# Performance work log

Measured on AMD Instinct MI355X. Metric: run time of the kernel, lower is better.

Reference implementation:

```python
import jax, jax.numpy as jnp
import numpy as np
from jax import lax

SPLINE_ORDER = 3  # default in KANLinear


def make_grid(in_features, grid_size, order=SPLINE_ORDER):
    # grid_range = [-1, 1], extended by spline_order knots on each side
    h = 2.0 / grid_size
    g = jnp.arange(-order, grid_size + order + 1, dtype=jnp.float32) * h - 1.0
    return jnp.broadcast_to(g, (in_features, g.shape[0]))  # (in, G)


def b_splines(x, grid, order=SPLINE_ORDER):
    # x: (N, in), grid: (in, G). Cox-de Boor recursion.
    x = x[..., None]  # (N, in, 1)
    bases = ((x >= grid[:, :-1]) & (x < grid[:, 1:])).astype(x.dtype)
    for k in range(1, order + 1):
        bases = ((x - grid[:, : -(k + 1)]) / (grid[:, k:-1] - grid[:, : -(k + 1)]) * bases[..., :-1]
                 + (grid[:, k + 1:] - x) / (grid[:, k + 1:] - grid[:, 1:-k]) * bases[..., 1:])
    return bases  # (N, in, grid_size + order)


def kan_conv(x, base_w, spline_w, scaler, grid_size, kernel, pad):
    # x: (B, C, H, W); base_w: (n_convs, K); spline_w: (n_convs, K, grid_size+order); scaler: (n_convs, K)
    B, C, H, W = x.shape
    kh, kw = kernel
    K = kh * kw
    if K == 1:
        p = x.reshape(-1, 1)  # (B*C*H*W, 1)
        Ho, Wo = H, W
    else:
        # patches: (B, C*K, Ho, Wo), feature dim ordered channel-major then (kh, kw)
        patches = lax.conv_general_dilated_patches(x, (kh, kw), (1, 1), [(pad, pad), (pad, pad)])
        Ho, Wo = patches.shape[2], patches.shape[3]
        p = patches.reshape(B, C, K, Ho, Wo).transpose(0, 1, 3, 4, 2).reshape(-1, K)
    grid = make_grid(K, grid_size)
    bases = b_splines(p, grid)  # (N, K, coef) -- shared across all n_convs kernels
    base = jnp.einsum('ni,ki->nk', jax.nn.silu(p), base_w)
    spl = jnp.einsum('nic,kic->nk', bases, spline_w * scaler[..., None])
    n_convs = base_w.shape[0]
    # channel ordering: each input channel expanded into n_convs outputs (channel-major)
    out = (base + spl).reshape(B, C, Ho, Wo, n_convs).transpose(0, 1, 4, 2, 3)
    return out.reshape(B, C * n_convs, Ho, Wo)


def setup_inputs() -> dict:
    key = jax.random.key(0)
    ks = jax.random.split(key, 12)
    B, C, H, W = 4, 3, 256, 256
    coef3 = 3 + SPLINE_ORDER  # grid_size=3 -> 6 spline coefficients
    coef5 = 5 + SPLINE_ORDER  # grid_size=5 (default, kan_conv6) -> 8
    s9 = 1.0 / np.sqrt(9.0)
    return {
        'x': jax.random.normal(ks[0], (B, C, H, W), jnp.float32),
        'base_w1': jax.random.normal(ks[1], (2, 9), jnp.float32) * s9,
        'spline_w1': jax.random.normal(ks[2], (2, 9, coef3), jnp.float32) * 0.1,
        'scaler1': 1.0 + 0.1 * jax.random.normal(ks[3], (2, 9), jnp.float32),
        'base_w2': jax.random.normal(ks[4], (2, 9), jnp.float32) * s9,
        'spline_w2': jax.random.normal(ks[5], (2, 9, coef3), jnp.float32) * 0.1,
        'scaler2': 1.0 + 0.1 * jax.random.normal(ks[6], (2, 9), jnp.float32),
        'conv_w': jax.random.normal(ks[7], (3, 12, 1, 1), jnp.float32) * (1.0 / np.sqrt(12.0)),
        'conv_b': jax.random.normal(ks[8], (3,), jnp.float32) * 0.01,
        'base_w6': jax.random.normal(ks[9], (1, 1), jnp.float32),
        'spline_w6': jax.random.normal(ks[10], (1, 1, coef5), jnp.float32) * 0.1,
        'scaler6': 1.0 + 0.1 * jax.random.normal(ks[11], (1, 1), jnp.float32),
    }


def reference(x, base_w1, spline_w1, scaler1, base_w2, spline_w2, scaler2,
              conv_w, conv_b, base_w6, spline_w6, scaler6):
    x = kan_conv(x, base_w1, spline_w1, scaler1, grid_size=3, kernel=(3, 3), pad=1)   # (B,6,H,W)
    x = kan_conv(x, base_w2, spline_w2, scaler2, grid_size=3, kernel=(3, 3), pad=1)   # (B,12,H,W)
    x = jnp.einsum('bchw,oc->bohw', x, conv_w[:, :, 0, 0]) + conv_b[None, :, None, None]  # 1x1 conv -> (B,3,H,W)
    return kan_conv(x, base_w6, spline_w6, scaler6, grid_size=5, kernel=(1, 1), pad=0)  # (B,3,H,W)
```

## Files before the change

### kernel.cpp

```cpp
#include <hip/hip_runtime.h>

#define TILE 16

__device__ __forceinline__ float2 kan_enc(float v, float g0, float invh, float tmax) {
    float g = v / (1.0f + __expf(-v));
    float T = (v - g0) * invh;
    float U = (T >= 0.0f && T < tmax) ? T : -1.0f;
    float2 r; r.x = g; r.y = U; return r;
}

__device__ __forceinline__ float poly_eval(float4 c, float w) {
    return ((c.w * w + c.z) * w + c.y) * w + c.x;
}

__global__ __launch_bounds__(256) void ZS_MKAN_72121090834671_kernel(
    const float* __restrict__ x,
    const float* __restrict__ base_w1, const float* __restrict__ spline_w1,
    const float* __restrict__ scaler1,
    const float* __restrict__ base_w2, const float* __restrict__ spline_w2,
    const float* __restrict__ scaler2,
    const float* __restrict__ conv_w, const float* __restrict__ conv_b,
    const float* __restrict__ base_w6, const float* __restrict__ spline_w6,
    const float* __restrict__ scaler6,
    float* __restrict__ out)
{
    __shared__ float2 encX[1200];
    __shared__ float2 encY[1944];
    __shared__ float4 coefL[2][2][9][10];
    __shared__ float4 coef6[12];
    __shared__ float  sbw[2][18];
    __shared__ float  scw[36], scb[3];
    __shared__ float  sb6;

    const int tid = threadIdx.x;
    const int tx0 = blockIdx.x * TILE;
    const int ty0 = blockIdx.y * TILE;
    const int b   = blockIdx.z;

    for (int e = tid; e < 360; e += 256) {
        int l = e / 180, r = e % 180, k = r / 90, r2 = r % 90, s = r2 / 10, si = r2 % 10;
        float4 v = make_float4(0.f, 0.f, 0.f, 0.f);
        if (si > 0) {
            const float* sw  = l ? spline_w2 : spline_w1;
            const float* scl = l ? scaler2   : scaler1;
            float sc = scl[k * 9 + s];
            int m = si - 1;
            float W[4];
            #pragma unroll
            for (int j = 0; j < 4; ++j) {
                int c = m - 3 + j;
                W[j] = (c >= 0 && c < 6) ? sw[(k * 9 + s) * 6 + c] * sc : 0.0f;
            }
            const float s6 = 1.0f / 6.0f;
            v.x = (W[0] + 4.0f * W[1] + W[2]) * s6;
            v.y = 3.0f * (W[2] - W[0]) * s6;
            v.z = (3.0f * W[0] - 6.0f * W[1] + 3.0f * W[2]) * s6;
            v.w = (W[3] - W[0] + 3.0f * (W[1] - W[2])) * s6;
        }
        coefL[l][k][s][si] = v;
    }
    if (tid < 12) {
        float4 v = make_float4(0.f, 0.f, 0.f, 0.f);
        if (tid > 0) {
            float sc = scaler6[0];
            int m = tid - 1;
            float W[4];
            #pragma unroll
            for (int j = 0; j < 4; ++j) {
                int c = m - 3 + j;
                W[j] = (c >= 0 && c < 8) ? spline_w6[c] * sc : 0.0f;
            }
            const float s6 = 1.0f / 6.0f;
            v.x = (W[0] + 4.0f * W[1] + W[2]) * s6;
            v.y = 3.0f * (W[2] - W[0]) * s6;
            v.z = (3.0f * W[0] - 6.0f * W[1] + 3.0f * W[2]) * s6;
            v.w = (W[3] - W[0] + 3.0f * (W[1] - W[2])) * s6;
        }
        coef6[tid] = v;
    }
    if (tid < 18) { sbw[0][tid] = base_w1[tid]; sbw[1][tid] = base_w2[tid]; }
    if (tid < 36) scw[tid] = conv_w[tid];
    if (tid < 3)  scb[tid] = conv_b[tid];
    if (tid == 0) sb6 = base_w6[0];

    for (int i = tid; i < 1200; i += 256) {
        int c = i / 400, r = i % 400, ly = r / 20, lx = r % 20;
        int gy = ty0 - 2 + ly, gx = tx0 - 2 + lx;
        float v = 0.0f;
        if ((unsigned)gy < 256u && (unsigned)gx < 256u)
            v = x[((b * 3 + c) * 256 + gy) * 256 + gx];
        encX[i] = kan_enc(v, -3.0f, 1.5f, 9.0f);
    }
    __syncthreads();

    for (int i = tid; i < 972; i += 256) {
        int c = i / 324, r = i % 324, ly = r / 18, lx = r % 18;
        float a0 = 0.0f, a1 = 0.0f;
        int base = c * 400 + ly * 20 + lx;
        #pragma unroll
        for (int s = 0; s < 9; ++s) {
            float2 t = encX[base + (s / 3) * 20 + (s % 3)];
            float mf = floorf(t.y);
            float w  = t.y - mf;
            int  si  = (int)mf + 1;
            a0 += t.x * sbw[0][s]     + poly_eval(coefL[0][0][s][si], w);
            a1 += t.x * sbw[0][9 + s] + poly_eval(coefL[0][1][s][si], w);
        }
        int gy = ty0 - 1 + ly, gx = tx0 - 1 + lx;
        if (!((unsigned)gy < 256u && (unsigned)gx < 256u)) { a0 = 0.0f; a1 = 0.0f; }
        encY[(c * 2 + 0) * 324 + r] = kan_enc(a0, -3.0f, 1.5f, 9.0f);
        encY[(c * 2 + 1) * 324 + r] = kan_enc(a1, -3.0f, 1.5f, 9.0f);
    }
    __syncthreads();

    const int ly = tid >> 4, lx = tid & 15;
    float z[12];
    #pragma unroll
    for (int c = 0; c < 6; ++c) {
        float a0 = 0.0f, a1 = 0.0f;
        int base = c * 324 + ly * 18 + lx;
        #pragma unroll
        for (int s = 0; s < 9; ++s) {
            float2 t = encY[base + (s / 3) * 18 + (s % 3)];
            float mf = floorf(t.y);
            float w  = t.y - mf;
            int  si  = (int)mf + 1;
            a0 += t.x * sbw[1][s]     + poly_eval(coefL[1][0][s][si], w);
            a1 += t.x * sbw[1][9 + s] + poly_eval(coefL[1][1][s][si], w);
        }
        z[2 * c]     = a0;
        z[2 * c + 1] = a1;
    }

    const int gy = ty0 + ly, gx = tx0 + lx;
    #pragma unroll
    for (int o = 0; o < 3; ++o) {
        float v = scb[o];
        #pragma unroll
        for (int c = 0; c < 12; ++c) v += scw[o * 12 + c] * z[c];
        float2 t = kan_enc(v, -2.2f, 2.5f, 11.0f);
        float mf = floorf(t.y);
        float w  = t.y - mf;
        int  si  = (int)mf + 1;
        out[((b * 3 + o) * 256 + gy) * 256 + gx] = t.x * sb6 + poly_eval(coef6[si], w);
    }
}

extern "C" void kernel_launch(void* const* d_in, const int* in_sizes, int n_in,
                              void* d_out, int out_size, void* d_ws, size_t ws_size,
                              hipStream_t stream) {
    (void)in_sizes; (void)n_in; (void)d_ws; (void)ws_size; (void)out_size;
    const float* x         = (const float*)d_in[0];
    const float* base_w1   = (const float*)d_in[1];
    const float* spline_w1 = (const float*)d_in[2];
    const float* scaler1   = (const float*)d_in[3];
    const float* base_w2   = (const float*)d_in[4];
    const float* spline_w2 = (const float*)d_in[5];
    const float* scaler2   = (const float*)d_in[6];
    const float* conv_w    = (const float*)d_in[7];
    const float* conv_b    = (const float*)d_in[8];
    const float* base_w6   = (const float*)d_in[9];
    const float* spline_w6 = (const float*)d_in[10];
    const float* scaler6   = (const float*)d_in[11];
    float* out = (float*)d_out;

    dim3 grid(256 / TILE, 256 / TILE, 4);
    dim3 block(256);
    ZS_MKAN_72121090834671_kernel<<<grid, block, 0, stream>>>(
        x, base_w1, spline_w1, scaler1, base_w2, spline_w2, scaler2,
        conv_w, conv_b, base_w6, spline_w6, scaler6, out);
}
```

Measured before the change: 26.27 us.

## Pack layer-2 spline coefficients as fp16 and interleave encoded channels in LDS

Layer-2 encoded activations for the two output channels of each input channel are stored together as one float4, so one LDS load serves both. The layer-2 cubic polynomial coefficients for both kernels are packed as half2 pairs into one uint4, so a single 16-byte LDS read fetches coefficients for two convs. The aim is fewer LDS transactions and a smaller LDS footprint in the hot second stage. The cost is fp16 rounding of the coefficients, which reduces accuracy, plus extra unpack instructions.

```diff
diff --git a/kernel.cpp b/kernel.cpp
--- a/kernel.cpp
+++ b/kernel.cpp
@@ -1,4 +1,5 @@
 #include <hip/hip_runtime.h>
+#include <hip/hip_fp16.h>
 
 #define TILE 16
 
@@ -6,11 +7,41 @@
     float g = v / (1.0f + __expf(-v));
     float T = (v - g0) * invh;
     float U = (T >= 0.0f && T < tmax) ? T : -1.0f;
-    float2 r; r.x = g; r.y = U; return r;
+    return make_float2(g, U);
 }
 
 __device__ __forceinline__ float poly_eval(float4 c, float w) {
     return ((c.w * w + c.z) * w + c.y) * w + c.x;
+}
+
+__device__ __forceinline__ float4 spline_poly(const float* __restrict__ sw, float sc,
+                                              int ncoef, int si) {
+    float4 v = make_float4(0.f, 0.f, 0.f, 0.f);
+    if (si > 0) {
+        int m = si - 1;
+        float W[4];
+        #pragma unroll
+        for (int j = 0; j < 4; ++j) {
+            int c = m - 3 + j;
+            W[j] = (c >= 0 && c < ncoef) ? sw[c] * sc : 0.0f;
+        }
+        const float s6 = 1.0f / 6.0f;
+        v.x = (W[0] + 4.0f * W[1] + W[2]) * s6;
+        v.y = 3.0f * (W[2] - W[0]) * s6;
+        v.z = (3.0f * W[0] - 6.0f * W[1] + 3.0f * W[2]) * s6;
+        v.w = (W[3] - W[0] + 3.0f * (W[1] - W[2])) * s6;
+    }
+    return v;
+}
+
+union H2U { __half2 h; unsigned u; };
+__device__ __forceinline__ unsigned pack_h2(float a, float b) {
+    H2U t; t.h = __halves2half2(__float2half_rn(a), __float2half_rn(b));
+    return t.u;
+}
+__device__ __forceinline__ float2 unpack_h2(unsigned u) {
+    H2U t; t.u = u;
+    return __half22float2(t.h);
 }
 
 __global__ __launch_bounds__(256) void ZS_MKAN_72121090834671_kernel(
@@ -25,8 +56,9 @@
     float* __restrict__ out)
 {
     __shared__ float2 encX[1200];
-    __shared__ float2 encY[1944];
-    __shared__ float4 coefL[2][2][9][10];
+    __shared__ float4 encY2[3][324];
+    __shared__ float4 coefL[2][9][10];
+    __shared__ uint4  coefH[9][10];
     __shared__ float4 coef6[12];
     __shared__ float  sbw[2][18];
     __shared__ float  scw[36], scb[3];
@@ -37,47 +69,21 @@
     const int ty0 = blockIdx.y * TILE;
     const int b   = blockIdx.z;
 
-    for (int e = tid; e < 360; e += 256) {
-        int l = e / 180, r = e % 180, k = r / 90, r2 = r % 90, s = r2 / 10, si = r2 % 10;
-        float4 v = make_float4(0.f, 0.f, 0.f, 0.f);
-        if (si > 0) {
-            const float* sw  = l ? spline_w2 : spline_w1;
-            const float* scl = l ? scaler2   : scaler1;
-            float sc = scl[k * 9 + s];
-            int m = si - 1;
-            float W[4];
-            #pragma unroll
-            for (int j = 0; j < 4; ++j) {
-                int c = m - 3 + j;
-                W[j] = (c >= 0 && c < 6) ? sw[(k * 9 + s) * 6 + c] * sc : 0.0f;
-            }
-            const float s6 = 1.0f / 6.0f;
-            v.x = (W[0] + 4.0f * W[1] + W[2]) * s6;
-            v.y = 3.0f * (W[2] - W[0]) * s6;
-            v.z = (3.0f * W[0] - 6.0f * W[1] + 3.0f * W[2]) * s6;
-            v.w = (W[3] - W[0] + 3.0f * (W[1] - W[2])) * s6;
-        }
-        coefL[l][k][s][si] = v;
+    for (int e = tid; e < 180; e += 256) {
+        int k = e / 90, r = e % 90, s = r / 10, si = r % 10;
+        coefL[k][s][si] = spline_poly(spline_w1 + (k * 9 + s) * 6,
+                                      scaler1[k * 9 + s], 6, si);
     }
-    if (tid < 12) {
-        float4 v = make_float4(0.f, 0.f, 0.f, 0.f);
-        if (tid > 0) {
-            float sc = scaler6[0];
-            int m = tid - 1;
-            float W[4];
-            #pragma unroll
-            for (int j = 0; j < 4; ++j) {
-                int c = m - 3 + j;
-                W[j] = (c >= 0 && c < 8) ? spline_w6[c] * sc : 0.0f;
-            }
-            const float s6 = 1.0f / 6.0f;
-            v.x = (W[0] + 4.0f * W[1] + W[2]) * s6;
-            v.y = 3.0f * (W[2] - W[0]) * s6;
-            v.z = (3.0f * W[0] - 6.0f * W[1] + 3.0f * W[2]) * s6;
-            v.w = (W[3] - W[0] + 3.0f * (W[1] - W[2])) * s6;
-        }
-        coef6[tid] = v;
+    for (int e = tid; e < 90; e += 256) {
+        int s = e / 10, si = e % 10;
+        float4 a = spline_poly(spline_w2 + s * 6,        scaler2[s],     6, si);
+        float4 c = spline_poly(spline_w2 + (9 + s) * 6,  scaler2[9 + s], 6, si);
+        uint4 q;
+        q.x = pack_h2(a.x, a.y); q.y = pack_h2(a.z, a.w);
+        q.z = pack_h2(c.x, c.y); q.w = pack_h2(c.z, c.w);
+        coefH[s][si] = q;
     }
+    if (tid < 12) coef6[tid] = spline_poly(spline_w6, scaler6[0], 8, tid);
     if (tid < 18) { sbw[0][tid] = base_w1[tid]; sbw[1][tid] = base_w2[tid]; }
     if (tid < 36) scw[tid] = conv_w[tid];
     if (tid < 3)  scb[tid] = conv_b[tid];
@@ -103,33 +109,49 @@
             float mf = floorf(t.y);
             float w  = t.y - mf;
             int  si  = (int)mf + 1;
-            a0 += t.x * sbw[0][s]     + poly_eval(coefL[0][0][s][si], w);
-            a1 += t.x * sbw[0][9 + s] + poly_eval(coefL[0][1][s][si], w);
+            a0 += t.x * sbw[0][s]     + poly_eval(coefL[0][s][si], w);
+            a1 += t.x * sbw[0][9 + s] + poly_eval(coefL[1][s][si], w);
         }
         int gy = ty0 - 1 + ly, gx = tx0 - 1 + lx;
         if (!((unsigned)gy < 256u && (unsigned)gx < 256u)) { a0 = 0.0f; a1 = 0.0f; }
-        encY[(c * 2 + 0) * 324 + r] = kan_enc(a0, -3.0f, 1.5f, 9.0f);
-        encY[(c * 2 + 1) * 324 + r] = kan_enc(a1, -3.0f, 1.5f, 9.0f);
+        float2 e0 = kan_enc(a0, -3.0f, 1.5f, 9.0f);
+        float2 e1 = kan_enc(a1, -3.0f, 1.5f, 9.0f);
+        encY2[c][r] = make_float4(e0.x, e0.y, e1.x, e1.y);
     }
     __syncthreads();
 
     const int ly = tid >> 4, lx = tid & 15;
     float z[12];
     #pragma unroll
-    for (int c = 0; c < 6; ++c) {
-        float a0 = 0.0f, a1 = 0.0f;
-        int base = c * 324 + ly * 18 + lx;
+    for (int c = 0; c < 3; ++c) {
+        float a00 = 0.0f, a01 = 0.0f, a10 = 0.0f, a11 = 0.0f;
         #pragma unroll
         for (int s = 0; s < 9; ++s) {
-            float2 t = encY[base + (s / 3) * 18 + (s % 3)];
-            float mf = floorf(t.y);
-            float w  = t.y - mf;
-            int  si  = (int)mf + 1;
-            a0 += t.x * sbw[1][s]     + poly_eval(coefL[1][0][s][si], w);
-            a1 += t.x * sbw[1][9 + s] + poly_eval(coefL[1][1][s][si], w);
+            float4 e = encY2[c][(ly + s / 3) * 18 + lx + (s % 3)];
+            float bw0 = sbw[1][s], bw1 = sbw[1][9 + s];
+            {
+                float mf = floorf(e.y);
+                float w  = e.y - mf;
+                int  si  = (int)mf + 1;
+                uint4 q = coefH[s][si];
+                float2 p0 = unpack_h2(q.x), p1 = unpack_h2(q.y);
+                float2 p2 = unpack_h2(q.z), p3 = unpack_h2(q.w);
+                a00 += e.x * bw0 + (((p1.y * w + p1.x) * w + p0.y) * w + p0.x);
+                a01 += e.x * bw1 + (((p3.y * w + p3.x) * w + p2.y) * w + p2.x);
+            }
+            {
+                float mf = floorf(e.w);
+                float w  = e.w - mf;
+                int  si  = (int)mf + 1;
+                uint4 q = coefH[s][si];
+                float2 p0 = unpack_h2(q.x), p1 = unpack_h2(q.y);
+                float2 p2 = unpack_h2(q.z), p3 = unpack_h2(q.w);
+                a10 += e.z * bw0 + (((p1.y * w + p1.x) * w + p0.y) * w + p0.x);
+                a11 += e.z * bw1 + (((p3.y * w + p3.x) * w + p2.y) * w + p2.x);
+            }
         }
-        z[2 * c]     = a0;
-        z[2 * c + 1] = a1;
+        z[4 * c + 0] = a00; z[4 * c + 1] = a01;
+        z[4 * c + 2] = a10; z[4 * c + 3] = a11;
     }
 
     const int gy = ty0 + ly, gx = tx0 + lx;
```

Result: slower. 27.43 us (+4.4%).
